# Optimization experiments

Hardware: AMD Instinct MI355X
Metric: run time of the kernel (lower is better)

The kernel has to match this reference:

```python
import jax, jax.numpy as jnp
import numpy as np

MAX_IT = 20
LAMBDA_ROF = 7.0
SIGMA = 1.0 / (7.0 * 0.01)
TAU = 0.01
THETA = 0.5
M, N = 4096, 4096


def _forward_weighted_gradient(x, w):
    # x: [1, M, N], w: [2, M, N] -> [2, M, N]
    x0 = x[0]
    gx = jnp.pad(x0[:, 1:] - x0[:, :-1], ((0, 0), (0, 1)))  # last col stays 0
    gy = jnp.pad(x0[1:, :] - x0[:-1, :], ((0, 1), (0, 0)))  # last row stays 0
    return jnp.stack([gx, gy]) * w


def _backward_weighted_divergence(y, w):
    # y, w: [2, M, N] -> [1, M, N]
    yw = w * y
    h, v = yw[0], yw[1]
    d_h = jnp.concatenate([h[:, :1], h[:, 1:-1] - h[:, :-2], -h[:, -2:-1]], axis=1)
    d_v = jnp.concatenate([v[:1, :], v[1:-1, :] - v[:-2, :], -v[-2:-1, :]], axis=0)
    return (d_h + d_v)[None]


def setup_inputs() -> dict:
    key = jax.random.key(0)
    k1, k2, k3 = jax.random.split(key, 3)
    img_obs = jax.random.uniform(k1, (1, M, N), dtype=jnp.float32)
    w = jax.random.uniform(k2, (2, M, N), dtype=jnp.float32)
    y0 = jax.random.uniform(k3, (2, M, N), dtype=jnp.float32)
    return {"img_obs": img_obs, "w": w, "y0": y0}


def reference(img_obs, w, y0):
    denom = 1.0 + LAMBDA_ROF * TAU

    def body(carry, _):
        x, x_tilde, y = carry
        # dual update + L-inf ball projection (prox == clip to [-1, 1])
        y = jnp.clip(y + SIGMA * _forward_weighted_gradient(x_tilde, w), -1.0, 1.0)
        x_old = x
        # primal update
        x = (x + TAU * _backward_weighted_divergence(y, w)
             + LAMBDA_ROF * TAU * img_obs) / denom
        # over-relaxation
        x_tilde = x + THETA * (x - x_old)
        return (x, x_tilde, y), None

    (x, x_tilde, y), _ = jax.lax.scan(body, (img_obs, img_obs, y0), None, length=MAX_IT)
    return x_tilde
```

## Files before the change

kernel.cpp:

```cpp
#include <hip/hip_runtime.h>


#define MM 4096
#define NN 4096
static constexpr size_t PP = (size_t)MM * NN;

static constexpr float SIGMA_F  = 14.285714285714286f;
static constexpr float TAU_F    = 0.01f;
static constexpr float THETA_F  = 0.5f;
static constexpr float LT_F     = 0.07f;
static constexpr float INV_DEN  = 1.0f / 1.07f;

typedef _Float16 h16;
typedef __attribute__((ext_vector_type(8))) _Float16 h16x8;
typedef __attribute__((ext_vector_type(4))) float f32x4;

#define TR 16
#define TC 128
#define BR 20
#define NSTRIP 18
#define LSW 152

__device__ __forceinline__ float clip1(float v) {
    return fminf(1.0f, fmaxf(-1.0f, v));
}

template<bool H>
__device__ __forceinline__ void gld8(const void* __restrict__ p, long idx, bool ok, float* o) {
    if (!ok) {
        #pragma unroll
        for (int e = 0; e < 8; ++e) o[e] = 0.f;
        return;
    }
    if constexpr (H) {
        h16x8 v = *reinterpret_cast<const h16x8*>(reinterpret_cast<const h16*>(p) + idx);
        #pragma unroll
        for (int e = 0; e < 8; ++e) o[e] = (float)v[e];
    } else {
        const float* q = reinterpret_cast<const float*>(p) + idx;
        f32x4 a = *reinterpret_cast<const f32x4*>(q);
        f32x4 b = *reinterpret_cast<const f32x4*>(q + 4);
        o[0]=a.x;o[1]=a.y;o[2]=a.z;o[3]=a.w;o[4]=b.x;o[5]=b.y;o[6]=b.z;o[7]=b.w;
    }
}

template<bool H>
__device__ __forceinline__ float gld1(const void* __restrict__ p, long idx, bool ok) {
    if (!ok) return 0.f;
    if constexpr (H) return (float)reinterpret_cast<const h16*>(p)[idx];
    else             return reinterpret_cast<const float*>(p)[idx];
}

__device__ __forceinline__ void lds8h(const h16* p, float* o) {
    h16x8 v = *reinterpret_cast<const h16x8*>(p);
    #pragma unroll
    for (int e = 0; e < 8; ++e) o[e] = (float)v[e];
}
__device__ __forceinline__ void lds8f(const float* p, float* o) {
    f32x4 a = *reinterpret_cast<const f32x4*>(p);
    f32x4 b = *reinterpret_cast<const f32x4*>(p + 4);
    o[0]=a.x;o[1]=a.y;o[2]=a.z;o[3]=a.w;o[4]=b.x;o[5]=b.y;o[6]=b.z;o[7]=b.w;
}

template<int MODE, bool WH, bool IH>
__global__ __launch_bounds__(256, 4)
void pd2(const h16* __restrict__ xprev, const h16* __restrict__ xcur,
         const void* __restrict__ yin, const void* __restrict__ w,
         const void* __restrict__ img,
         h16* __restrict__ xo1, h16* __restrict__ xo2, h16* __restrict__ yo,
         h16* __restrict__ w_h, h16* __restrict__ img_h,
         float* __restrict__ out)
{
    constexpr bool FIRST = (MODE == 0);
    constexpr bool LAST  = (MODE == 2);
    constexpr bool WRH = (!FIRST) && WH;
    constexpr bool IRH = (!FIRST) && IH;

    __shared__ float sXT[BR][LSW];
    __shared__ h16   sX [BR][LSW];
    __shared__ h16   sY0[BR][LSW];
    __shared__ h16   sY1[BR][LSW];

    const int tid = threadIdx.x;
    const int bi0 = blockIdx.y * TR;
    const int bj0 = blockIdx.x * TC;

    for (int t = tid; t < BR * NSTRIP; t += 256) {
        const int r = t / NSTRIP, s = t - r * NSTRIP;
        const int gi = bi0 - 2 + r;
        const int gj = bj0 - 8 + 8 * s;
        const long idx = (long)gi * NN + gj;
        const bool ok = (gi >= 0) & (gi < MM) & (gj >= 0) & (gj < NN);
        const int l = 8 * s;
        float xt8[8]; h16x8 xh;
        if constexpr (FIRST) {
            float v[8];
            gld8<false>(img, idx, ok, v);
            #pragma unroll
            for (int e = 0; e < 8; ++e) { xt8[e] = v[e]; xh[e] = (h16)v[e]; }
        } else {
            float xp[8], xc[8];
            gld8<true>(xprev, idx, ok, xp);
            gld8<true>(xcur,  idx, ok, xc);
            #pragma unroll
            for (int e = 0; e < 8; ++e) {
                xt8[e] = fmaf(THETA_F, xc[e] - xp[e], xc[e]);
                xh[e]  = (h16)xc[e];
            }
        }
        #pragma unroll
        for (int e = 0; e < 8; ++e) sXT[r][l + e] = xt8[e];
        *reinterpret_cast<h16x8*>(&sX[r][l]) = xh;
    }
    __syncthreads();

    for (int t = tid; t < 19 * NSTRIP; t += 256) {
        const int r = t / NSTRIP, s = t - r * NSTRIP;
        const int gi = bi0 - 2 + r;
        const int gj0 = bj0 - 8 + 8 * s;
        const long idx = (long)gi * NN + gj0;
        const bool ok = (gi >= 0) & (gi < MM) & (gj0 >= 0) & (gj0 < NN);
        const int l = 8 * s;

        float y0v[8], y1v[8], w0v[8], w1v[8];
        gld8<!FIRST>(yin, idx, ok, y0v);
        gld8<!FIRST>(yin, (long)PP + idx, ok, y1v);
        gld8<WRH>(w, idx, ok, w0v);
        gld8<WRH>(w, (long)PP + idx, ok, w1v);

        float xtC[8], xtD[8];
        lds8f(&sXT[r][l], xtC);
        const float xtR = sXT[r][l + 8];
        lds8f(&sXT[r + 1][l], xtD);

        h16x8 y0s, y1s;
        #pragma unroll
        for (int e = 0; e < 8; ++e) {
            const int gj = gj0 + e;
            const float xtr = (e < 7) ? xtC[e + 1] : xtR;
            const float gx = (gj < NN - 1) ? (xtr - xtC[e]) : 0.f;
            const float gy = (gi < MM - 1) ? (xtD[e] - xtC[e]) : 0.f;
            y0s[e] = (h16)clip1(fmaf(SIGMA_F * gx, w0v[e], y0v[e]));
            y1s[e] = (h16)clip1(fmaf(SIGMA_F * gy, w1v[e], y1v[e]));
        }
        *reinterpret_cast<h16x8*>(&sY0[r][l]) = y0s;
        *reinterpret_cast<h16x8*>(&sY1[r][l]) = y1s;

        if constexpr (FIRST && WH) {
            if (r >= 2 && r <= 17 && s >= 1 && s <= 16) {
                h16x8 a, b;
                #pragma unroll
                for (int e = 0; e < 8; ++e) { a[e] = (h16)w0v[e]; b[e] = (h16)w1v[e]; }
                *reinterpret_cast<h16x8*>(&w_h[idx]) = a;
                *reinterpret_cast<h16x8*>(&w_h[PP + idx]) = b;
            }
        }
    }
    __syncthreads();

    for (int t = tid; t < 18 * NSTRIP; t += 256) {
        const int r = 1 + t / NSTRIP, s = t % NSTRIP;
        const int gi = bi0 - 2 + r;
        const int gj0 = bj0 - 8 + 8 * s;
        const long idx = (long)gi * NN + gj0;
        const bool ok  = (gi >= 0) & (gi < MM) & (gj0 >= 0) & (gj0 < NN);
        const bool okU = (gi >= 1) & (gj0 >= 0) & (gj0 < NN);
        const int l = 8 * s;

        float y0C[8], y1C[8], y1U[8];
        lds8h(&sY0[r][l], y0C);
        lds8h(&sY1[r][l], y1C);
        lds8h(&sY1[r - 1][l], y1U);
        const int lm1 = (l > 0) ? (l - 1) : 0;
        const float y0L = (float)sY0[r][lm1];

        float w0C[8], w1C[8], w1U[8];
        gld8<WRH>(w, idx, ok, w0C);
        gld8<WRH>(w, (long)PP + idx, ok, w1C);
        gld8<WRH>(w, (long)PP + idx - NN, okU, w1U);
        const float w0L = gld1<WRH>(w, idx - 1, ok & (gj0 > 0));

        float gim[8];
        gld8<IRH>(img, idx, ok, gim);

        float xc[8];
        if constexpr (FIRST) {
            #pragma unroll
            for (int e = 0; e < 8; ++e) xc[e] = gim[e];
        } else {
            lds8h(&sX[r][l], xc);
        }

        float h[8];
        #pragma unroll
        for (int e = 0; e < 8; ++e) {
            const int gj = gj0 + e;
            h[e] = (gj < NN - 1) ? w0C[e] * y0C[e] : 0.f;
        }
        const float hL = w0L * y0L;
        float dh[8];
        dh[0] = h[0] - hL;
        #pragma unroll
        for (int e = 1; e < 8; ++e) dh[e] = h[e] - h[e - 1];

        const bool notbot = (gi < MM - 1);
        h16x8 xh; float xt1[8];
        #pragma unroll
        for (int e = 0; e < 8; ++e) {
            const float vC = notbot ? w1C[e] * y1C[e] : 0.f;
            const float vU = w1U[e] * y1U[e];
            const float xv = (xc[e] + TAU_F * (dh[e] + vC - vU) + LT_F * gim[e]) * INV_DEN;
            const h16 hh = (h16)xv;
            const float xvh = (float)hh;
            xh[e] = hh;
            xt1[e] = fmaf(THETA_F, xvh - xc[e], xvh);
        }
        *reinterpret_cast<h16x8*>(&sX[r][l]) = xh;
        #pragma unroll
        for (int e = 0; e < 8; ++e) sXT[r][l + e] = xt1[e];

        if constexpr (!LAST) {
            if (r >= 2 && r <= 17 && s >= 1 && s <= 16)
                *reinterpret_cast<h16x8*>(&xo1[idx]) = xh;
        }
        if constexpr (FIRST && IH) {
            if (r >= 2 && r <= 17 && s >= 1 && s <= 16) {
                h16x8 g8;
                #pragma unroll
                for (int e = 0; e < 8; ++e) g8[e] = (h16)gim[e];
                *reinterpret_cast<h16x8*>(&img_h[idx]) = g8;
            }
        }
    }
    __syncthreads();

    for (int t = tid; t < 17 * 17; t += 256) {
        const int r = 1 + t / 17, s = t % 17;
        const int gi = bi0 - 2 + r;
        const int gj0 = bj0 - 8 + 8 * s;
        const long idx = (long)gi * NN + gj0;
        const bool ok = (gi >= 0) & (gi < MM) & (gj0 >= 0) & (gj0 < NN);
        const int l = 8 * s;

        float w0v[8], w1v[8];
        gld8<WRH>(w, idx, ok, w0v);
        gld8<WRH>(w, (long)PP + idx, ok, w1v);

        float xtC[8], xtD[8];
        lds8f(&sXT[r][l], xtC);
        const float xtR = sXT[r][l + 8];
        lds8f(&sXT[r + 1][l], xtD);

        float y0p[8], y1p[8];
        lds8h(&sY0[r][l], y0p);
        lds8h(&sY1[r][l], y1p);

        h16x8 y0s, y1s;
        #pragma unroll
        for (int e = 0; e < 8; ++e) {
            const int gj = gj0 + e;
            const float xtr = (e < 7) ? xtC[e + 1] : xtR;
            const float gx = (gj < NN - 1) ? (xtr - xtC[e]) : 0.f;
            const float gy = (gi < MM - 1) ? (xtD[e] - xtC[e]) : 0.f;
            y0s[e] = (h16)clip1(fmaf(SIGMA_F * gx, w0v[e], y0p[e]));
            y1s[e] = (h16)clip1(fmaf(SIGMA_F * gy, w1v[e], y1p[e]));
        }
        *reinterpret_cast<h16x8*>(&sY0[r][l]) = y0s;
        *reinterpret_cast<h16x8*>(&sY1[r][l]) = y1s;
        if constexpr (!LAST) {
            if (r >= 2 && s >= 1) {
                *reinterpret_cast<h16x8*>(&yo[idx]) = y0s;
                *reinterpret_cast<h16x8*>(&yo[PP + idx]) = y1s;
            }
        }
    }
    __syncthreads();

    {
        const int r = 2 + (tid >> 4);
        const int s = 1 + (tid & 15);
        const int gi = bi0 - 2 + r;
        const int gj0 = bj0 - 8 + 8 * s;
        const long idx = (long)gi * NN + gj0;
        const int l = 8 * s;

        float y0C[8], y1C[8], y1U[8];
        lds8h(&sY0[r][l], y0C);
        lds8h(&sY1[r][l], y1C);
        lds8h(&sY1[r - 1][l], y1U);
        const float y0L = (float)sY0[r][l - 1];

        float w0C[8], w1C[8], w1U[8];
        gld8<WRH>(w, idx, true, w0C);
        gld8<WRH>(w, (long)PP + idx, true, w1C);
        gld8<WRH>(w, (long)PP + idx - NN, gi > 0, w1U);
        const float w0L = gld1<WRH>(w, idx - 1, gj0 > 0);

        float gim[8];
        gld8<IRH>(img, idx, true, gim);

        float xc1[8];
        lds8h(&sX[r][l], xc1);

        float h[8];
        #pragma unroll
        for (int e = 0; e < 8; ++e) {
            const int gj = gj0 + e;
            h[e] = (gj < NN - 1) ? w0C[e] * y0C[e] : 0.f;
        }
        const float hL = w0L * y0L;
        float dh[8];
        dh[0] = h[0] - hL;
        #pragma unroll
        for (int e = 1; e < 8; ++e) dh[e] = h[e] - h[e - 1];

        const bool notbot = (gi < MM - 1);
        if constexpr (!LAST) {
            h16x8 xh;
            #pragma unroll
            for (int e = 0; e < 8; ++e) {
                const float vC = notbot ? w1C[e] * y1C[e] : 0.f;
                const float vU = w1U[e] * y1U[e];
                const float xv = (xc1[e] + TAU_F * (dh[e] + vC - vU) + LT_F * gim[e]) * INV_DEN;
                xh[e] = (h16)xv;
            }
            *reinterpret_cast<h16x8*>(&xo2[idx]) = xh;
        } else {
            float o[8];
            #pragma unroll
            for (int e = 0; e < 8; ++e) {
                const float vC = notbot ? w1C[e] * y1C[e] : 0.f;
                const float vU = w1U[e] * y1U[e];
                const float xv = (xc1[e] + TAU_F * (dh[e] + vC - vU) + LT_F * gim[e]) * INV_DEN;
                o[e] = fmaf(THETA_F, xv - xc1[e], xv);
            }
            f32x4 a, b;
            a.x = o[0]; a.y = o[1]; a.z = o[2]; a.w = o[3];
            b.x = o[4]; b.y = o[5]; b.z = o[6]; b.w = o[7];
            *reinterpret_cast<f32x4*>(&out[idx]) = a;
            *reinterpret_cast<f32x4*>(&out[idx + 4]) = b;
        }
    }
}

template<bool WH, bool IH>
static void run_seq(hipStream_t s, const float* img, const float* w, const float* y0,
                    h16* const* xb, h16* yA, h16* yB, h16* w_h, h16* img_h, float* out)
{
    const dim3 grid(NN / TC, MM / TR);
    const dim3 block(256);
    for (int k = 0; k < 10; ++k) {
        const h16* xp = xb[(2 * k + 3) & 3];
        const h16* xc = xb[(2 * k) & 3];
        h16* xo1 = xb[(2 * k + 1) & 3];
        h16* xo2 = xb[(2 * k + 2) & 3];
        const void* yin = (k == 0) ? (const void*)y0
                                   : ((k & 1) ? (const void*)yA : (const void*)yB);
        h16* yo = (k & 1) ? yB : yA;
        const void* wp = (k == 0) ? (const void*)w
                                  : (WH ? (const void*)w_h : (const void*)w);
        const void* ip = (k == 0) ? (const void*)img
                                  : (IH ? (const void*)img_h : (const void*)img);
        if (k == 0)
            pd2<0, WH, IH><<<grid, block, 0, s>>>(xp, xc, yin, wp, ip, xo1, xo2, yo, w_h, img_h, out);
        else if (k == 9)
            pd2<2, WH, IH><<<grid, block, 0, s>>>(xp, xc, yin, wp, ip, xo1, xo2, yo, w_h, img_h, out);
        else
            pd2<1, WH, IH><<<grid, block, 0, s>>>(xp, xc, yin, wp, ip, xo1, xo2, yo, w_h, img_h, out);
    }
}

extern "C" void kernel_launch(void* const* d_in, const int* in_sizes, int n_in,
                              void* d_out, int out_size, void* d_ws, size_t ws_size,
                              hipStream_t stream) {
    const float* img = (const float*)d_in[0];
    const float* w   = (const float*)d_in[1];
    const float* y0  = (const float*)d_in[2];

    h16* base = (h16*)d_ws;
    h16* xb[4] = { base, base + PP, base + 2 * PP, base + 3 * PP };
    h16* yA = base + 4 * PP;

    const size_t planes = ws_size / (PP * sizeof(h16));
    const bool WH = planes >= 8;
    const bool IH = (planes >= 9) || (planes == 7);
    h16* w_h   = WH ? base + 6 * PP : nullptr;
    h16* img_h = IH ? (WH ? base + 8 * PP : base + 6 * PP) : nullptr;

    h16* yB = (h16*)d_out;
    float* out = (float*)d_out;

    if (WH && IH)      run_seq<true,  true >(stream, img, w, y0, xb, yA, yB, w_h, img_h, out);
    else if (WH)       run_seq<true,  false>(stream, img, w, y0, xb, yA, yB, w_h, img_h, out);
    else if (IH)       run_seq<false, true >(stream, img, w, y0, xb, yA, yB, w_h, img_h, out);
    else               run_seq<false, false>(stream, img, w, y0, xb, yA, yB, w_h, img_h, out);
}
```

Baseline: 1.706 ms.

## Register-resident one-thread-per-strip tile with shared-memory weights for fused two-step kernel

Restructures the fused two-iteration kernel so each of 320 threads owns one 8-wide strip of a 20x128 haloed tile (16x112 interior) and keeps x, y, w and img in registers across all four phases. Weights are staged once into shared memory as fp16 instead of being re-read from global memory in every phase, and the left/up neighbour values come from shared memory. This removes repeated global loads of w and img and the strided loop indexing. In exchange the interior is narrower, so halo overhead and redundant recompute grow, the grid no longer divides the image width evenly, and register pressure rises.

```diff
diff --git a/kernel.cpp b/kernel.cpp
--- a/kernel.cpp
+++ b/kernel.cpp
@@ -15,11 +15,10 @@
 typedef __attribute__((ext_vector_type(8))) _Float16 h16x8;
 typedef __attribute__((ext_vector_type(4))) float f32x4;
 
-#define TR 16
-#define TC 128
-#define BR 20
-#define NSTRIP 18
-#define LSW 152
+#define TIR 16
+#define TIC 112
+#define RRW 20
+#define LSW 144
 
 __device__ __forceinline__ float clip1(float v) {
     return fminf(1.0f, fmaxf(-1.0f, v));
@@ -44,13 +43,6 @@
     }
 }
 
-template<bool H>
-__device__ __forceinline__ float gld1(const void* __restrict__ p, long idx, bool ok) {
-    if (!ok) return 0.f;
-    if constexpr (H) return (float)reinterpret_cast<const h16*>(p)[idx];
-    else             return reinterpret_cast<const float*>(p)[idx];
-}
-
 __device__ __forceinline__ void lds8h(const h16* p, float* o) {
     h16x8 v = *reinterpret_cast<const h16x8*>(p);
     #pragma unroll
@@ -63,7 +55,7 @@
 }
 
 template<int MODE, bool WH, bool IH>
-__global__ __launch_bounds__(256, 4)
+__global__ __launch_bounds__(320, 4)
 void pd2(const h16* __restrict__ xprev, const h16* __restrict__ xcur,
          const void* __restrict__ yin, const void* __restrict__ w,
          const void* __restrict__ img,
@@ -76,252 +68,181 @@
     constexpr bool WRH = (!FIRST) && WH;
     constexpr bool IRH = (!FIRST) && IH;
 
-    __shared__ float sXT[BR][LSW];
-    __shared__ h16   sX [BR][LSW];
-    __shared__ h16   sY0[BR][LSW];
-    __shared__ h16   sY1[BR][LSW];
+    __shared__ float sXT[RRW][LSW];
+    __shared__ h16   sY0[RRW][LSW];
+    __shared__ h16   sY1[RRW][LSW];
+    __shared__ h16   sW0[RRW][LSW];
+    __shared__ h16   sW1[RRW][LSW];
 
     const int tid = threadIdx.x;
-    const int bi0 = blockIdx.y * TR;
-    const int bj0 = blockIdx.x * TC;
-
-    for (int t = tid; t < BR * NSTRIP; t += 256) {
-        const int r = t / NSTRIP, s = t - r * NSTRIP;
-        const int gi = bi0 - 2 + r;
-        const int gj = bj0 - 8 + 8 * s;
-        const long idx = (long)gi * NN + gj;
-        const bool ok = (gi >= 0) & (gi < MM) & (gj >= 0) & (gj < NN);
-        const int l = 8 * s;
-        float xt8[8]; h16x8 xh;
-        if constexpr (FIRST) {
-            float v[8];
-            gld8<false>(img, idx, ok, v);
-            #pragma unroll
-            for (int e = 0; e < 8; ++e) { xt8[e] = v[e]; xh[e] = (h16)v[e]; }
-        } else {
-            float xp[8], xc[8];
-            gld8<true>(xprev, idx, ok, xp);
-            gld8<true>(xcur,  idx, ok, xc);
-            #pragma unroll
-            for (int e = 0; e < 8; ++e) {
-                xt8[e] = fmaf(THETA_F, xc[e] - xp[e], xc[e]);
-                xh[e]  = (h16)xc[e];
-            }
-        }
-        #pragma unroll
-        for (int e = 0; e < 8; ++e) sXT[r][l + e] = xt8[e];
-        *reinterpret_cast<h16x8*>(&sX[r][l]) = xh;
-    }
-    __syncthreads();
-
-    for (int t = tid; t < 19 * NSTRIP; t += 256) {
-        const int r = t / NSTRIP, s = t - r * NSTRIP;
-        const int gi = bi0 - 2 + r;
-        const int gj0 = bj0 - 8 + 8 * s;
-        const long idx = (long)gi * NN + gj0;
-        const bool ok = (gi >= 0) & (gi < MM) & (gj0 >= 0) & (gj0 < NN);
-        const int l = 8 * s;
-
-        float y0v[8], y1v[8], w0v[8], w1v[8];
-        gld8<!FIRST>(yin, idx, ok, y0v);
-        gld8<!FIRST>(yin, (long)PP + idx, ok, y1v);
+    const int r = tid >> 4;
+    const int s = tid & 15;
+    const int l = 8 * s;
+    const int L = l + 8;
+    const int gi  = blockIdx.y * TIR - 2 + r;
+    const int gj0 = blockIdx.x * TIC - 8 + l;
+    const long idx = (long)gi * NN + gj0;
+    const bool ok = (gi >= 0) & (gi < MM) & (gj0 >= 0) & (gj0 < NN);
+    const bool interior = (r >= 2) & (r <= 17) & (s >= 1) & (s <= 14) & (gj0 < NN);
+    const bool notbot = gi < MM - 1;
+
+    float xcv[8], y0v[8], y1v[8], w0v[8], w1v[8], gim[8], xtv[8];
+
+    if constexpr (FIRST) {
+        gld8<false>(img, idx, ok, gim);
+        gld8<false>(yin, idx, ok, y0v);
+        gld8<false>(yin, (long)PP + idx, ok, y1v);
+        gld8<false>(w, idx, ok, w0v);
+        gld8<false>(w, (long)PP + idx, ok, w1v);
+        #pragma unroll
+        for (int e = 0; e < 8; ++e) { xcv[e] = gim[e]; xtv[e] = gim[e]; }
+    } else {
+        float xpv[8];
+        gld8<true>(xprev, idx, ok, xpv);
+        gld8<true>(xcur,  idx, ok, xcv);
+        gld8<IRH>(img, idx, ok, gim);
+        gld8<true>(yin, idx, ok, y0v);
+        gld8<true>(yin, (long)PP + idx, ok, y1v);
         gld8<WRH>(w, idx, ok, w0v);
         gld8<WRH>(w, (long)PP + idx, ok, w1v);
-
-        float xtC[8], xtD[8];
-        lds8f(&sXT[r][l], xtC);
-        const float xtR = sXT[r][l + 8];
-        lds8f(&sXT[r + 1][l], xtD);
-
-        h16x8 y0s, y1s;
+        #pragma unroll
+        for (int e = 0; e < 8; ++e) xtv[e] = fmaf(THETA_F, xcv[e] - xpv[e], xcv[e]);
+    }
+
+    #pragma unroll
+    for (int e = 0; e < 8; ++e) sXT[r][L + e] = xtv[e];
+    {
+        h16x8 t0, t1;
+        #pragma unroll
+        for (int e = 0; e < 8; ++e) { t0[e] = (h16)w0v[e]; t1[e] = (h16)w1v[e]; }
+        *reinterpret_cast<h16x8*>(&sW0[r][L]) = t0;
+        *reinterpret_cast<h16x8*>(&sW1[r][L]) = t1;
+        if constexpr (FIRST && WH) {
+            if (interior) {
+                *reinterpret_cast<h16x8*>(&w_h[idx]) = t0;
+                *reinterpret_cast<h16x8*>(&w_h[PP + idx]) = t1;
+            }
+        }
+    }
+    if constexpr (FIRST && IH) {
+        if (interior) {
+            h16x8 tg;
+            #pragma unroll
+            for (int e = 0; e < 8; ++e) tg[e] = (h16)gim[e];
+            *reinterpret_cast<h16x8*>(&img_h[idx]) = tg;
+        }
+    }
+    if (s == 0) {
+        #pragma unroll
+        for (int e = 0; e < 8; ++e) { sY0[r][e] = (h16)0.f; sW0[r][e] = (h16)0.f; }
+    }
+    if (s == 15) {
+        #pragma unroll
+        for (int e = 0; e < 8; ++e) sXT[r][136 + e] = 0.f;
+    }
+    __syncthreads();
+
+    if (r <= 18) {
+        float xtD[8];
+        const float xtR = sXT[r][L + 8];
+        lds8f(&sXT[r + 1][L], xtD);
+        h16x8 t0, t1;
         #pragma unroll
         for (int e = 0; e < 8; ++e) {
-            const int gj = gj0 + e;
-            const float xtr = (e < 7) ? xtC[e + 1] : xtR;
-            const float gx = (gj < NN - 1) ? (xtr - xtC[e]) : 0.f;
-            const float gy = (gi < MM - 1) ? (xtD[e] - xtC[e]) : 0.f;
-            y0s[e] = (h16)clip1(fmaf(SIGMA_F * gx, w0v[e], y0v[e]));
-            y1s[e] = (h16)clip1(fmaf(SIGMA_F * gy, w1v[e], y1v[e]));
-        }
-        *reinterpret_cast<h16x8*>(&sY0[r][l]) = y0s;
-        *reinterpret_cast<h16x8*>(&sY1[r][l]) = y1s;
-
-        if constexpr (FIRST && WH) {
-            if (r >= 2 && r <= 17 && s >= 1 && s <= 16) {
-                h16x8 a, b;
-                #pragma unroll
-                for (int e = 0; e < 8; ++e) { a[e] = (h16)w0v[e]; b[e] = (h16)w1v[e]; }
-                *reinterpret_cast<h16x8*>(&w_h[idx]) = a;
-                *reinterpret_cast<h16x8*>(&w_h[PP + idx]) = b;
+            const float xr = (e < 7) ? xtv[e + 1] : xtR;
+            const float gx = (gj0 + e < NN - 1) ? (xr - xtv[e]) : 0.f;
+            const float gy = notbot ? (xtD[e] - xtv[e]) : 0.f;
+            t0[e] = (h16)clip1(fmaf(SIGMA_F * gx, w0v[e], y0v[e]));
+            t1[e] = (h16)clip1(fmaf(SIGMA_F * gy, w1v[e], y1v[e]));
+            y0v[e] = (float)t0[e];
+            y1v[e] = (float)t1[e];
+        }
+        *reinterpret_cast<h16x8*>(&sY0[r][L]) = t0;
+        *reinterpret_cast<h16x8*>(&sY1[r][L]) = t1;
+    }
+    __syncthreads();
+
+    if (r >= 1 && r <= 18) {
+        const float y0L = (float)sY0[r][L - 1];
+        const float w0L = (float)sW0[r][L - 1];
+        float y1U[8], w1U[8];
+        lds8h(&sY1[r - 1][L], y1U);
+        lds8h(&sW1[r - 1][L], w1U);
+        float hh[8];
+        #pragma unroll
+        for (int e = 0; e < 8; ++e)
+            hh[e] = (gj0 + e < NN - 1) ? w0v[e] * y0v[e] : 0.f;
+        float dh[8];
+        dh[0] = hh[0] - w0L * y0L;
+        #pragma unroll
+        for (int e = 1; e < 8; ++e) dh[e] = hh[e] - hh[e - 1];
+        h16x8 xh;
+        #pragma unroll
+        for (int e = 0; e < 8; ++e) {
+            const float vC = notbot ? w1v[e] * y1v[e] : 0.f;
+            const float vU = w1U[e] * y1U[e];
+            const float xv = (xcv[e] + TAU_F * (dh[e] + vC - vU) + LT_F * gim[e]) * INV_DEN;
+            const h16 hx = (h16)xv;
+            const float xvh = (float)hx;
+            xh[e] = hx;
+            xtv[e] = fmaf(THETA_F, xvh - xcv[e], xvh);
+            xcv[e] = xvh;
+        }
+        #pragma unroll
+        for (int e = 0; e < 8; ++e) sXT[r][L + e] = xtv[e];
+        if constexpr (!LAST) {
+            if (interior) *reinterpret_cast<h16x8*>(&xo1[idx]) = xh;
+        }
+    }
+    __syncthreads();
+
+    if (r >= 1 && r <= 17) {
+        float xtD[8];
+        const float xtR = sXT[r][L + 8];
+        lds8f(&sXT[r + 1][L], xtD);
+        h16x8 t0, t1;
+        #pragma unroll
+        for (int e = 0; e < 8; ++e) {
+            const float xr = (e < 7) ? xtv[e + 1] : xtR;
+            const float gx = (gj0 + e < NN - 1) ? (xr - xtv[e]) : 0.f;
+            const float gy = notbot ? (xtD[e] - xtv[e]) : 0.f;
+            t0[e] = (h16)clip1(fmaf(SIGMA_F * gx, w0v[e], y0v[e]));
+            t1[e] = (h16)clip1(fmaf(SIGMA_F * gy, w1v[e], y1v[e]));
+            y0v[e] = (float)t0[e];
+            y1v[e] = (float)t1[e];
+        }
+        *reinterpret_cast<h16x8*>(&sY0[r][L]) = t0;
+        *reinterpret_cast<h16x8*>(&sY1[r][L]) = t1;
+        if constexpr (!LAST) {
+            if (interior) {
+                *reinterpret_cast<h16x8*>(&yo[idx]) = t0;
+                *reinterpret_cast<h16x8*>(&yo[PP + idx]) = t1;
             }
         }
     }
     __syncthreads();
 
-    for (int t = tid; t < 18 * NSTRIP; t += 256) {
-        const int r = 1 + t / NSTRIP, s = t % NSTRIP;
-        const int gi = bi0 - 2 + r;
-        const int gj0 = bj0 - 8 + 8 * s;
-        const long idx = (long)gi * NN + gj0;
-        const bool ok  = (gi >= 0) & (gi < MM) & (gj0 >= 0) & (gj0 < NN);
-        const bool okU = (gi >= 1) & (gj0 >= 0) & (gj0 < NN);
-        const int l = 8 * s;
-
-        float y0C[8], y1C[8], y1U[8];
-        lds8h(&sY0[r][l], y0C);
-        lds8h(&sY1[r][l], y1C);
-        lds8h(&sY1[r - 1][l], y1U);
-        const int lm1 = (l > 0) ? (l - 1) : 0;
-        const float y0L = (float)sY0[r][lm1];
-
-        float w0C[8], w1C[8], w1U[8];
-        gld8<WRH>(w, idx, ok, w0C);
-        gld8<WRH>(w, (long)PP + idx, ok, w1C);
-        gld8<WRH>(w, (long)PP + idx - NN, okU, w1U);
-        const float w0L = gld1<WRH>(w, idx - 1, ok & (gj0 > 0));
-
-        float gim[8];
-        gld8<IRH>(img, idx, ok, gim);
-
-        float xc[8];
-        if constexpr (FIRST) {
-            #pragma unroll
-            for (int e = 0; e < 8; ++e) xc[e] = gim[e];
-        } else {
-            lds8h(&sX[r][l], xc);
-        }
-
-        float h[8];
-        #pragma unroll
-        for (int e = 0; e < 8; ++e) {
-            const int gj = gj0 + e;
-            h[e] = (gj < NN - 1) ? w0C[e] * y0C[e] : 0.f;
-        }
-        const float hL = w0L * y0L;
+    if (interior) {
+        const float y0L = (float)sY0[r][L - 1];
+        const float w0L = (float)sW0[r][L - 1];
+        float y1U[8], w1U[8];
+        lds8h(&sY1[r - 1][L], y1U);
+        lds8h(&sW1[r - 1][L], w1U);
+        float hh[8];
+        #pragma unroll
+        for (int e = 0; e < 8; ++e)
+            hh[e] = (gj0 + e < NN - 1) ? w0v[e] * y0v[e] : 0.f;
         float dh[8];
-        dh[0] = h[0] - hL;
-        #pragma unroll
-        for (int e = 1; e < 8; ++e) dh[e] = h[e] - h[e - 1];
-
-        const bool notbot = (gi < MM - 1);
-        h16x8 xh; float xt1[8];
-        #pragma unroll
-        for (int e = 0; e < 8; ++e) {
-            const float vC = notbot ? w1C[e] * y1C[e] : 0.f;
-            const float vU = w1U[e] * y1U[e];
-            const float xv = (xc[e] + TAU_F * (dh[e] + vC - vU) + LT_F * gim[e]) * INV_DEN;
-            const h16 hh = (h16)xv;
-            const float xvh = (float)hh;
-            xh[e] = hh;
-            xt1[e] = fmaf(THETA_F, xvh - xc[e], xvh);
-        }
-        *reinterpret_cast<h16x8*>(&sX[r][l]) = xh;
-        #pragma unroll
-        for (int e = 0; e < 8; ++e) sXT[r][l + e] = xt1[e];
-
-        if constexpr (!LAST) {
-            if (r >= 2 && r <= 17 && s >= 1 && s <= 16)
-                *reinterpret_cast<h16x8*>(&xo1[idx]) = xh;
-        }
-        if constexpr (FIRST && IH) {
-            if (r >= 2 && r <= 17 && s >= 1 && s <= 16) {
-                h16x8 g8;
-                #pragma unroll
-                for (int e = 0; e < 8; ++e) g8[e] = (h16)gim[e];
-                *reinterpret_cast<h16x8*>(&img_h[idx]) = g8;
-            }
-        }
-    }
-    __syncthreads();
-
-    for (int t = tid; t < 17 * 17; t += 256) {
-        const int r = 1 + t / 17, s = t % 17;
-        const int gi = bi0 - 2 + r;
-        const int gj0 = bj0 - 8 + 8 * s;
-        const long idx = (long)gi * NN + gj0;
-        const bool ok = (gi >= 0) & (gi < MM) & (gj0 >= 0) & (gj0 < NN);
-        const int l = 8 * s;
-
-        float w0v[8], w1v[8];
-        gld8<WRH>(w, idx, ok, w0v);
-        gld8<WRH>(w, (long)PP + idx, ok, w1v);
-
-        float xtC[8], xtD[8];
-        lds8f(&sXT[r][l], xtC);
-        const float xtR = sXT[r][l + 8];
-        lds8f(&sXT[r + 1][l], xtD);
-
-        float y0p[8], y1p[8];
-        lds8h(&sY0[r][l], y0p);
-        lds8h(&sY1[r][l], y1p);
-
-        h16x8 y0s, y1s;
-        #pragma unroll
-        for (int e = 0; e < 8; ++e) {
-            const int gj = gj0 + e;
-            const float xtr = (e < 7) ? xtC[e + 1] : xtR;
-            const float gx = (gj < NN - 1) ? (xtr - xtC[e]) : 0.f;
-            const float gy = (gi < MM - 1) ? (xtD[e] - xtC[e]) : 0.f;
-            y0s[e] = (h16)clip1(fmaf(SIGMA_F * gx, w0v[e], y0p[e]));
-            y1s[e] = (h16)clip1(fmaf(SIGMA_F * gy, w1v[e], y1p[e]));
-        }
-        *reinterpret_cast<h16x8*>(&sY0[r][l]) = y0s;
-        *reinterpret_cast<h16x8*>(&sY1[r][l]) = y1s;
-        if constexpr (!LAST) {
-            if (r >= 2 && s >= 1) {
-                *reinterpret_cast<h16x8*>(&yo[idx]) = y0s;
-                *reinterpret_cast<h16x8*>(&yo[PP + idx]) = y1s;
-            }
-        }
-    }
-    __syncthreads();
-
-    {
-        const int r = 2 + (tid >> 4);
-        const int s = 1 + (tid & 15);
-        const int gi = bi0 - 2 + r;
-        const int gj0 = bj0 - 8 + 8 * s;
-        const long idx = (long)gi * NN + gj0;
-        const int l = 8 * s;
-
-        float y0C[8], y1C[8], y1U[8];
-        lds8h(&sY0[r][l], y0C);
-        lds8h(&sY1[r][l], y1C);
-        lds8h(&sY1[r - 1][l], y1U);
-        const float y0L = (float)sY0[r][l - 1];
-
-        float w0C[8], w1C[8], w1U[8];
-        gld8<WRH>(w, idx, true, w0C);
-        gld8<WRH>(w, (long)PP + idx, true, w1C);
-        gld8<WRH>(w, (long)PP + idx - NN, gi > 0, w1U);
-        const float w0L = gld1<WRH>(w, idx - 1, gj0 > 0);
-
-        float gim[8];
-        gld8<IRH>(img, idx, true, gim);
-
-        float xc1[8];
-        lds8h(&sX[r][l], xc1);
-
-        float h[8];
-        #pragma unroll
-        for (int e = 0; e < 8; ++e) {
-            const int gj = gj0 + e;
-            h[e] = (gj < NN - 1) ? w0C[e] * y0C[e] : 0.f;
-        }
-        const float hL = w0L * y0L;
-        float dh[8];
-        dh[0] = h[0] - hL;
-        #pragma unroll
-        for (int e = 1; e < 8; ++e) dh[e] = h[e] - h[e - 1];
-
-        const bool notbot = (gi < MM - 1);
+        dh[0] = hh[0] - w0L * y0L;
+        #pragma unroll
+        for (int e = 1; e < 8; ++e) dh[e] = hh[e] - hh[e - 1];
         if constexpr (!LAST) {
             h16x8 xh;
             #pragma unroll
             for (int e = 0; e < 8; ++e) {
-                const float vC = notbot ? w1C[e] * y1C[e] : 0.f;
+                const float vC = notbot ? w1v[e] * y1v[e] : 0.f;
                 const float vU = w1U[e] * y1U[e];
-                const float xv = (xc1[e] + TAU_F * (dh[e] + vC - vU) + LT_F * gim[e]) * INV_DEN;
+                const float xv = (xcv[e] + TAU_F * (dh[e] + vC - vU) + LT_F * gim[e]) * INV_DEN;
                 xh[e] = (h16)xv;
             }
             *reinterpret_cast<h16x8*>(&xo2[idx]) = xh;
@@ -329,10 +250,10 @@
             float o[8];
             #pragma unroll
             for (int e = 0; e < 8; ++e) {
-                const float vC = notbot ? w1C[e] * y1C[e] : 0.f;
+                const float vC = notbot ? w1v[e] * y1v[e] : 0.f;
                 const float vU = w1U[e] * y1U[e];
-                const float xv = (xc1[e] + TAU_F * (dh[e] + vC - vU) + LT_F * gim[e]) * INV_DEN;
-                o[e] = fmaf(THETA_F, xv - xc1[e], xv);
+                const float xv = (xcv[e] + TAU_F * (dh[e] + vC - vU) + LT_F * gim[e]) * INV_DEN;
+                o[e] = fmaf(THETA_F, xv - xcv[e], xv);
             }
             f32x4 a, b;
             a.x = o[0]; a.y = o[1]; a.z = o[2]; a.w = o[3];
@@ -347,8 +268,8 @@
 static void run_seq(hipStream_t s, const float* img, const float* w, const float* y0,
                     h16* const* xb, h16* yA, h16* yB, h16* w_h, h16* img_h, float* out)
 {
-    const dim3 grid(NN / TC, MM / TR);
-    const dim3 block(256);
+    const dim3 grid((NN + TIC - 1) / TIC, MM / TIR);
+    const dim3 block(320);
     for (int k = 0; k < 10; ++k) {
         const h16* xp = xb[(2 * k + 3) & 3];
         const h16* xc = xb[(2 * k) & 3];
```

After: 1.535 ms. 1.11x faster.
